# Performance work log

Hardware: AMD Instinct MI355X
Metric: run time of the kernel (lower is better)

Reference implementation:

```python
import jax, jax.numpy as jnp
import numpy as np

N_NODES = 100000
N_EDGES = 800000
IN_DIM, HID, OUT_DIM = 128, 96, 32
BN_EPS = 1e-5


def gcn_conv(x, W, b, src, dst, n):
    # PyG GCNConv: linear -> symmetric-normalized aggregation (with self-loops) -> +bias
    h = x @ W  # [N, out]
    sl = jnp.arange(n)
    s = jnp.concatenate([src, sl])
    d = jnp.concatenate([dst, sl])
    deg = jax.ops.segment_sum(jnp.ones(s.shape[0], dtype=x.dtype), d, num_segments=n)
    dinv = jnp.where(deg > 0, jax.lax.rsqrt(deg), 0.0)
    norm = dinv[s] * dinv[d]  # [E+N]
    out = jax.ops.segment_sum(norm[:, None] * h[s], d, num_segments=n)
    return out + b


def batchnorm(x, gamma, beta):
    mu = jnp.mean(x, axis=0)
    var = jnp.var(x, axis=0)
    return gamma * (x - mu) * jax.lax.rsqrt(var + BN_EPS) + beta


def setup_inputs() -> dict:
    key = jax.random.key(0)
    ks = jax.random.split(key, 8)
    glorot = lambda k, fi, fo: jax.random.normal(k, (fi, fo), jnp.float32) * np.sqrt(2.0 / (fi + fo))
    return {
        "x": jax.random.normal(ks[0], (N_NODES, IN_DIM), jnp.float32),
        "edge_index": jax.random.randint(ks[1], (2, N_EDGES), 0, N_NODES, jnp.int64),
        "W1": glorot(ks[2], IN_DIM, HID), "b1": jnp.zeros((HID,), jnp.float32),
        "W2": glorot(ks[3], HID, HID), "b2": jnp.zeros((HID,), jnp.float32),
        "W3": glorot(ks[4], HID, OUT_DIM), "b3": jnp.zeros((OUT_DIM,), jnp.float32),
        "g1": jnp.ones((HID,), jnp.float32), "be1": jnp.zeros((HID,), jnp.float32),
        "g2": jnp.ones((HID,), jnp.float32), "be2": jnp.zeros((HID,), jnp.float32),
    }


def reference(x, edge_index, W1, b1, W2, b2, W3, b3, g1, be1, g2, be2):
    src, dst = edge_index[0], edge_index[1]
    n = x.shape[0]
    h = gcn_conv(x, W1, b1, src, dst, n)
    h = jax.nn.relu(batchnorm(h, g1, be1))  # dropout is identity in eval
    h = gcn_conv(h, W2, b2, src, dst, n)
    h = jax.nn.relu(batchnorm(h, g2, be2))
    h = gcn_conv(h, W3, b3, src, dst, n)
    return jax.nn.log_softmax(h, axis=-1)
```

## Files before the change

### kernel.cpp

```cpp
#include <hip/hip_runtime.h>
#include <hip/hip_fp16.h>
#include <cstddef>

#define NN 100000
#define NE 800000
#define DIN 128
#define HID 96
#define DOUT 32
static constexpr float BN_EPS = 1e-5f;
#define SCAN_NB ((NN + 255) / 256)

typedef unsigned short u16;
typedef unsigned int u32;

__device__ __forceinline__ float b2f(u32 lo16) {
    union { u32 u; float f; } c; c.u = lo16 << 16; return c.f;
}
__device__ __forceinline__ u16 f2b(float f) {
    union { float f; u32 u; } c; c.f = f;
    return (u16)((c.u + 0x7FFFu + ((c.u >> 16) & 1u)) >> 16);
}
__device__ __forceinline__ u32 pack_edge(int s, float w) {
    __half h = __float2half(w);
    return ((u32)s << 15) | (u32)__half_as_ushort(h);
}
__device__ __forceinline__ int edge_src(u32 pk) { return (int)(pk >> 15); }
__device__ __forceinline__ float edge_wt(u32 pk) {
    return __half2float(__ushort_as_half((u16)(pk & 0x7FFFu)));
}


__global__ void k_init(int* __restrict__ deg) {
    int i = blockIdx.x * 256 + threadIdx.x;
    if (i < NN) deg[i] = 0;
}

__global__ __launch_bounds__(256) void k_scan1(const int* __restrict__ deg,
                                               int* __restrict__ row_start,
                                               int* __restrict__ blksum,
                                               float* __restrict__ dinv) {
    __shared__ int lds[256];
    int t = threadIdx.x;
    int i = blockIdx.x * 256 + t;
    int v = (i < NN) ? deg[i] : 0;
    if (i < NN) dinv[i] = rsqrtf((float)(v + 1));
    lds[t] = v;
    __syncthreads();
#pragma unroll
    for (int off = 1; off < 256; off <<= 1) {
        int add = (t >= off) ? lds[t - off] : 0;
        __syncthreads();
        lds[t] += add;
        __syncthreads();
    }
    if (i < NN) row_start[i] = lds[t] - v;
    if (t == 255) blksum[blockIdx.x] = lds[255];
}

__global__ __launch_bounds__(512) void k_scan2(int* __restrict__ blksum,
                                               int* __restrict__ row_start,
                                               float* __restrict__ meta) {
    __shared__ int lds[512];
    int t = threadIdx.x;
    if (t < 384) meta[t] = 0.f;
    int v = (t < SCAN_NB) ? blksum[t] : 0;
    lds[t] = v;
    __syncthreads();
#pragma unroll
    for (int off = 1; off < 512; off <<= 1) {
        int add = (t >= off) ? lds[t - off] : 0;
        __syncthreads();
        lds[t] += add;
        __syncthreads();
    }
    if (t < SCAN_NB) blksum[t] = lds[t] - v;
    if (t == 511) row_start[NN] = lds[511];
}

__global__ __launch_bounds__(256) void k_scan3(int* __restrict__ row_start,
                                               const int* __restrict__ blksum) {
    int i = blockIdx.x * 256 + threadIdx.x;
    if (i < NN) row_start[i] += blksum[blockIdx.x];
}

__global__ void k_scatter(const int* __restrict__ src, const int* __restrict__ dst,
                          const int* __restrict__ row_start,
                          const int* __restrict__ rank,
                          const float* __restrict__ dinv,
                          u32* __restrict__ ewt) {
    int e = blockIdx.x * blockDim.x + threadIdx.x;
    if (e < NE) {
        int d = dst[e];
        int p = row_start[d] + rank[e];
        int s = src[e];
        ewt[p] = pack_edge(s, dinv[s]);
    }
}

template <int KD, int ND, bool FUSE, typename XT>
__device__ __forceinline__ void gemm_body(int bid, const XT* __restrict__ X,
                                          const float* __restrict__ W,
                                          u16* __restrict__ Z,
                                          const float* __restrict__ bnA,
                                          const float* __restrict__ bnC, int M) {
    constexpr int BK = 32;
    constexpr int CT = 16;
    constexpr int CPT = ND / CT;
    constexpr int RPT = 8;
    constexpr int XS = 132;
    __shared__ float Xs[BK * XS];
    __shared__ float Ws[BK * ND];
    __shared__ float As[KD], Cs[KD];

    int tid = threadIdx.x;
    if (FUSE && tid < KD) { As[tid] = bnA[tid]; Cs[tid] = bnC[tid]; }
    int row0 = bid * 128;
    int ct = tid % CT, rt = tid / CT;
    float acc[RPT][CPT];
#pragma unroll
    for (int r = 0; r < RPT; ++r)
#pragma unroll
        for (int c = 0; c < CPT; ++c) acc[r][c] = 0.f;

    for (int k0 = 0; k0 < KD; k0 += BK) {
        __syncthreads();
        if constexpr (sizeof(XT) == 4) {
#pragma unroll
            for (int pass = 0; pass < 4; ++pass) {
                int r = pass * 32 + (tid >> 3);
                int kq = (tid & 7) * 4;
                int grow = row0 + r;
                float4 v = make_float4(0.f, 0.f, 0.f, 0.f);
                if (grow < M) v = *(const float4*)&X[(size_t)grow * KD + k0 + kq];
                if (FUSE) {
                    v.x = fmaxf(fmaf(As[k0 + kq + 0], v.x, Cs[k0 + kq + 0]), 0.f);
                    v.y = fmaxf(fmaf(As[k0 + kq + 1], v.y, Cs[k0 + kq + 1]), 0.f);
                    v.z = fmaxf(fmaf(As[k0 + kq + 2], v.z, Cs[k0 + kq + 2]), 0.f);
                    v.w = fmaxf(fmaf(As[k0 + kq + 3], v.w, Cs[k0 + kq + 3]), 0.f);
                }
                Xs[(kq + 0) * XS + r] = v.x;
                Xs[(kq + 1) * XS + r] = v.y;
                Xs[(kq + 2) * XS + r] = v.z;
                Xs[(kq + 3) * XS + r] = v.w;
            }
        } else {
#pragma unroll
            for (int pass = 0; pass < 2; ++pass) {
                int r = pass * 64 + (tid >> 2);
                int kq = (tid & 3) * 8;
                int grow = row0 + r;
                uint4 v = make_uint4(0, 0, 0, 0);
                if (grow < M) v = *(const uint4*)&X[(size_t)grow * KD + k0 + kq];
                u32 w[4] = {v.x, v.y, v.z, v.w};
#pragma unroll
                for (int q = 0; q < 4; ++q) {
                    float lo = b2f(w[q] & 0xFFFFu);
                    float hi = b2f(w[q] >> 16);
                    if (FUSE) {
                        lo = fmaxf(fmaf(As[k0 + kq + 2 * q + 0], lo, Cs[k0 + kq + 2 * q + 0]), 0.f);
                        hi = fmaxf(fmaf(As[k0 + kq + 2 * q + 1], hi, Cs[k0 + kq + 2 * q + 1]), 0.f);
                    }
                    Xs[(kq + 2 * q + 0) * XS + r] = lo;
                    Xs[(kq + 2 * q + 1) * XS + r] = hi;
                }
            }
        }
#pragma unroll
        for (int f = tid; f < BK * ND / 4; f += 256) {
            int kk = f / (ND / 4);
            int c4 = (f % (ND / 4)) * 4;
            *(float4*)&Ws[kk * ND + c4] = *(const float4*)&W[(size_t)(k0 + kk) * ND + c4];
        }
        __syncthreads();
#pragma unroll
        for (int kk = 0; kk < BK; ++kk) {
            float4 x0 = *(const float4*)&Xs[kk * XS + rt * 8];
            float4 x1 = *(const float4*)&Xs[kk * XS + rt * 8 + 4];
            float xr[RPT] = {x0.x, x0.y, x0.z, x0.w, x1.x, x1.y, x1.z, x1.w};
            float wc[CPT];
#pragma unroll
            for (int c = 0; c < CPT; ++c) wc[c] = Ws[kk * ND + ct * CPT + c];
#pragma unroll
            for (int r = 0; r < RPT; ++r)
#pragma unroll
                for (int c = 0; c < CPT; ++c) acc[r][c] = fmaf(xr[r], wc[c], acc[r][c]);
        }
    }
#pragma unroll
    for (int r = 0; r < RPT; ++r) {
        int grow = row0 + rt * RPT + r;
        if (grow < M) {
#pragma unroll
            for (int c = 0; c < CPT; c += 2) {
                u32 pk = (u32)f2b(acc[r][c]) | ((u32)f2b(acc[r][c + 1]) << 16);
                *(u32*)&Z[(size_t)grow * ND + ct * CPT + c] = pk;
            }
        }
    }
}

template <int KD, int ND, bool FUSE, typename XT>
__global__ __launch_bounds__(256) void k_gemm(const XT* __restrict__ X,
                                              const float* __restrict__ W,
                                              u16* __restrict__ Z,
                                              const float* __restrict__ bnA,
                                              const float* __restrict__ bnC, int M) {
    gemm_body<KD, ND, FUSE, XT>(blockIdx.x, X, W, Z, bnA, bnC, M);
}

__global__ __launch_bounds__(256) void k_gemm1_hist(const float* __restrict__ X,
                                                    const float* __restrict__ W,
                                                    u16* __restrict__ Z, int M,
                                                    int gemm_blocks,
                                                    const int* __restrict__ dst,
                                                    int* __restrict__ deg,
                                                    int* __restrict__ rank) {
    if ((int)blockIdx.x < gemm_blocks) {
        gemm_body<DIN, HID, false, float>(blockIdx.x, X, W, Z, nullptr, nullptr, M);
    } else {
        int e = ((int)blockIdx.x - gemm_blocks) * 256 + (int)threadIdx.x;
        if (e < NE) rank[e] = atomicAdd(&deg[dst[e]], 1);
    }
}

__global__ __launch_bounds__(256) void k_agg96(const u16* __restrict__ Z,
                                               u16* __restrict__ H,
                                               const float* __restrict__ bias,
                                               const int* __restrict__ row_start,
                                               const u32* __restrict__ ewt,
                                               const float* __restrict__ dinv,
                                               float* __restrict__ gsum,
                                               float* __restrict__ gsq) {
    __shared__ float ssum[96], ssq[96];
    int tid = threadIdx.x;
    if (tid < 96) { ssum[tid] = 0.f; ssq[tid] = 0.f; }
    __syncthreads();
    int wid = tid >> 6, lane = tid & 63;
    bool act = lane < 48;
    int l = act ? lane : 47;
    const u32* zu = (const u32*)Z;
    float b0 = bias[2 * l], b1 = bias[2 * l + 1];
    float lsum0 = 0.f, lsq0 = 0.f, lsum1 = 0.f, lsq1 = 0.f;
    const int stride = gridDim.x * 4;

    int n = blockIdx.x * 4 + wid;
    int e0 = 0, e1 = 0;
    u32 pr = 0;
    if (n < NN) {
        e0 = row_start[n]; e1 = row_start[n + 1];
        if (e0 + lane < e1) pr = ewt[e0 + lane];
    }
    while (n < NN) {
        int n2 = n + stride;
        int e0n = 0, e1n = 0;
        if (n2 < NN) { e0n = row_start[n2]; e1n = row_start[n2 + 1]; }

        float dn = dinv[n];
        u32 uself = zu[(size_t)n * 48 + l];
        float a0a = dn * b2f(uself & 0xFFFFu);
        float a1a = dn * b2f(uself >> 16);
        float a0b = 0.f, a1b = 0.f;

        u32 plv = pr;

        u32 prn = 0;
        if (n2 < NN && e0n + lane < e1n) prn = ewt[e0n + lane];

        int m = e1 - e0;
        if (m <= 64) {
            int K = (m + 7) >> 3;
            u32 uA[8], uB[8];
            float wA[8], wB[8];
            {
#pragma unroll
                for (int q = 0; q < 8; ++q) {
                    bool v = q < m;
                    u32 pk = __shfl(plv, v ? q : 0);
                    wA[q] = v ? edge_wt(pk) : 0.f;
                    uA[q] = zu[(size_t)edge_src(pk) * 48 + l];
                }
            }
            for (int c = 0; c < K; ++c) {
                if ((c & 1) == 0) {
                    if (c + 1 < K) {
#pragma unroll
                        for (int q = 0; q < 8; ++q) {
                            int j = (c + 1) * 8 + q;
                            bool v = j < m;
                            u32 pk = __shfl(plv, v ? j : 0);
                            wB[q] = v ? edge_wt(pk) : 0.f;
                            uB[q] = zu[(size_t)edge_src(pk) * 48 + l];
                        }
                    }
#pragma unroll
                    for (int q = 0; q < 8; q += 2) {
                        a0a = fmaf(wA[q], b2f(uA[q] & 0xFFFFu), a0a);
                        a1a = fmaf(wA[q], b2f(uA[q] >> 16), a1a);
                        a0b = fmaf(wA[q + 1], b2f(uA[q + 1] & 0xFFFFu), a0b);
                        a1b = fmaf(wA[q + 1], b2f(uA[q + 1] >> 16), a1b);
                    }
                } else {
                    if (c + 1 < K) {
#pragma unroll
                        for (int q = 0; q < 8; ++q) {
                            int j = (c + 1) * 8 + q;
                            bool v = j < m;
                            u32 pk = __shfl(plv, v ? j : 0);
                            wA[q] = v ? edge_wt(pk) : 0.f;
                            uA[q] = zu[(size_t)edge_src(pk) * 48 + l];
                        }
                    }
#pragma unroll
                    for (int q = 0; q < 8; q += 2) {
                        a0a = fmaf(wB[q], b2f(uB[q] & 0xFFFFu), a0a);
                        a1a = fmaf(wB[q], b2f(uB[q] >> 16), a1a);
                        a0b = fmaf(wB[q + 1], b2f(uB[q + 1] & 0xFFFFu), a0b);
                        a1b = fmaf(wB[q + 1], b2f(uB[q + 1] >> 16), a1b);
                    }
                }
            }
        } else {
            u32 cw = plv;
            for (int eb = e0; eb < e1; eb += 64) {
                if (eb != e0) {
                    int idx = eb + lane;
                    cw = (idx < e1) ? ewt[idx] : 0;
                }
                int mm = e1 - eb; if (mm > 64) mm = 64;
                for (int j = 0; j < mm; ++j) {
                    u32 pk = __shfl(cw, j);
                    float w = edge_wt(pk);
                    u32 u = zu[(size_t)edge_src(pk) * 48 + l];
                    a0a = fmaf(w, b2f(u & 0xFFFFu), a0a);
                    a1a = fmaf(w, b2f(u >> 16), a1a);
                }
            }
        }
        float h0 = fmaf(dn, a0a + a0b, b0);
        float h1 = fmaf(dn, a1a + a1b, b1);
        if (act) {
            u32 pk = (u32)f2b(h0) | ((u32)f2b(h1) << 16);
            ((u32*)H)[(size_t)n * 48 + l] = pk;
            lsum0 += h0; lsq0 = fmaf(h0, h0, lsq0);
            lsum1 += h1; lsq1 = fmaf(h1, h1, lsq1);
        }
        n = n2; e0 = e0n; e1 = e1n; pr = prn;
    }
    if (act) {
        atomicAdd(&ssum[2 * l], lsum0); atomicAdd(&ssq[2 * l], lsq0);
        atomicAdd(&ssum[2 * l + 1], lsum1); atomicAdd(&ssq[2 * l + 1], lsq1);
    }
    __syncthreads();
    if (tid < 96) { atomicAdd(&gsum[tid], ssum[tid]); atomicAdd(&gsq[tid], ssq[tid]); }
}

__global__ void k_bncoef(const float* __restrict__ gsum, const float* __restrict__ gsq,
                         const float* __restrict__ g, const float* __restrict__ be,
                         float* __restrict__ bnA, float* __restrict__ bnC) {
    int c = threadIdx.x;
    if (c < 96) {
        float mean = gsum[c] * (1.f / NN);
        float var = gsq[c] * (1.f / NN) - mean * mean;
        float inv = rsqrtf(var + BN_EPS);
        float a = g[c] * inv;
        bnA[c] = a;
        bnC[c] = fmaf(-a, mean, be[c]);
    }
}

__global__ __launch_bounds__(256) void k_agg32_lsm(const u16* __restrict__ Z,
                                                   float* __restrict__ Out,
                                                   const float* __restrict__ bias,
                                                   const int* __restrict__ row_start,
                                                   const u32* __restrict__ ewt,
                                                   const float* __restrict__ dinv) {
    int tid = threadIdx.x;
    int wid = tid >> 6, lane = tid & 63;
    int g = lane >> 4, sl = lane & 15;
    const u32* zu = (const u32*)Z;
    float b0 = bias[2 * sl], b1 = bias[2 * sl + 1];
    int stride = gridDim.x * 16;
    for (int n0 = (blockIdx.x * 4 + wid) * 4; n0 < NN; n0 += stride) {
        int n = n0 + g;
        bool vn = n < NN;
        float dn = vn ? dinv[n] : 0.f;
        u32 uself = vn ? zu[(size_t)n * 16 + sl] : 0;
        float a0a = dn * b2f(uself & 0xFFFFu);
        float a1a = dn * b2f(uself >> 16);
        float a0b = 0.f, a1b = 0.f;
        int e0 = vn ? row_start[n] : 0, e1 = vn ? row_start[n + 1] : 0;
        for (int eb = e0; eb < e1; eb += 16) {
            int m = e1 - eb; if (m > 16) m = 16;
            int idx = eb + sl;
            u32 plv = (idx < e1) ? ewt[idx] : 0;
            u32 u_[16]; float w_[16];
#pragma unroll
            for (int q = 0; q < 16; ++q) {
                bool v = q < m;
                u32 pk = __shfl(plv, v ? q : 0, 16);
                w_[q] = v ? edge_wt(pk) : 0.f;
                u_[q] = zu[(size_t)edge_src(pk) * 16 + sl];
            }
#pragma unroll
            for (int q = 0; q < 16; q += 2) {
                a0a = fmaf(w_[q], b2f(u_[q] & 0xFFFFu), a0a);
                a1a = fmaf(w_[q], b2f(u_[q] >> 16), a1a);
                a0b = fmaf(w_[q + 1], b2f(u_[q + 1] & 0xFFFFu), a0b);
                a1b = fmaf(w_[q + 1], b2f(u_[q + 1] >> 16), a1b);
            }
        }
        float v0 = fmaf(dn, a0a + a0b, b0);
        float v1 = fmaf(dn, a1a + a1b, b1);
        float mx = fmaxf(v0, v1);
#pragma unroll
        for (int off = 8; off; off >>= 1) mx = fmaxf(mx, __shfl_xor(mx, off, 16));
        float ex = __expf(v0 - mx) + __expf(v1 - mx);
#pragma unroll
        for (int off = 8; off; off >>= 1) ex += __shfl_xor(ex, off, 16);
        float lse = mx + __logf(ex);
        if (vn) {
            float2 o = make_float2(v0 - lse, v1 - lse);
            *(float2*)&Out[(size_t)n * 32 + 2 * sl] = o;
        }
    }
}


extern "C" void kernel_launch(void* const* d_in, const int* in_sizes, int n_in,
                              void* d_out, int out_size, void* d_ws, size_t ws_size,
                              hipStream_t stream) {
    const float* x  = (const float*)d_in[0];
    const int* ei   = (const int*)d_in[1];
    const float* W1 = (const float*)d_in[2];
    const float* b1 = (const float*)d_in[3];
    const float* W2 = (const float*)d_in[4];
    const float* b2 = (const float*)d_in[5];
    const float* W3 = (const float*)d_in[6];
    const float* b3 = (const float*)d_in[7];
    const float* g1 = (const float*)d_in[8];
    const float* be1 = (const float*)d_in[9];
    const float* g2 = (const float*)d_in[10];
    const float* be2 = (const float*)d_in[11];
    float* out = (float*)d_out;

    const int* src = ei;
    const int* dst = ei + NE;

    char* p = (char*)d_ws;
    size_t off = 0;
    auto take = [&](size_t bytes) {
        char* r = p + off;
        off = (off + bytes + 255) & ~(size_t)255;
        return r;
    };
    float* dinv      = (float*)take(NN * 4);
    int*   deg       = (int*)take(NN * 4);
    int*   row_start = (int*)take((NN + 1) * 4);
    int*   blksum    = (int*)take(SCAN_NB * 4);
    int*   rank      = (int*)take((size_t)NE * 4);
    u32*   ewt       = (u32*)take((size_t)NE * 4);
    float* meta      = (float*)take(768 * 4);
    u16*   bufA      = (u16*)take((size_t)NN * HID * 2);
    u16*   bufB      = (u16*)take((size_t)NN * HID * 2);

    float* sum1 = meta + 0,   *sq1 = meta + 96;
    float* sum2 = meta + 192, *sq2 = meta + 288;
    float* bnA1 = meta + 384, *bnC1 = meta + 480;
    float* bnA2 = meta + 576, *bnC2 = meta + 672;

    const int EB = (NE + 255) / 256;
    const int VB = (NN + 255) / 256;
    const int GB = (NN + 127) / 128;
    const int AB = 2048;

    k_init<<<VB, 256, 0, stream>>>(deg);
    k_gemm1_hist<<<GB + EB, 256, 0, stream>>>(x, W1, bufA, NN, GB, dst, deg, rank);
    k_scan1<<<SCAN_NB, 256, 0, stream>>>(deg, row_start, blksum, dinv);
    k_scan2<<<1, 512, 0, stream>>>(blksum, row_start, meta);
    k_scan3<<<SCAN_NB, 256, 0, stream>>>(row_start, blksum);
    k_scatter<<<EB, 256, 0, stream>>>(src, dst, row_start, rank, dinv, ewt);

    k_agg96<<<AB, 256, 0, stream>>>(bufA, bufB, b1, row_start, ewt, dinv, sum1, sq1);
    k_bncoef<<<1, 128, 0, stream>>>(sum1, sq1, g1, be1, bnA1, bnC1);

    k_gemm<HID, HID, true, u16><<<GB, 256, 0, stream>>>(bufB, W2, bufA, bnA1, bnC1, NN);
    k_agg96<<<AB, 256, 0, stream>>>(bufA, bufB, b2, row_start, ewt, dinv, sum2, sq2);
    k_bncoef<<<1, 128, 0, stream>>>(sum2, sq2, g2, be2, bnA2, bnC2);

    k_gemm<HID, DOUT, true, u16><<<GB, 256, 0, stream>>>(bufB, W3, bufA, bnA2, bnC2, NN);
    k_agg32_lsm<<<AB, 256, 0, stream>>>(bufA, out, b3, row_start, ewt, dinv);

    (void)in_sizes; (void)n_in; (void)out_size; (void)ws_size;
}
```

Baseline: 427.8 us.

## Fuse scan finalize into scatter, use nontemporal gather loads, chunk agg32 loop

Merges the third scan pass and the edge scatter into one launch, which writes finalized row offsets into a separate buffer while the scatter adds the block prefix itself. Edge-list and feature gathers in the aggregation kernels become nontemporal loads, meant to reduce cache pollution. The 32-wide aggregation now gathers in chunks of 8 with a dynamic trip count rather than a fixed 16-way unroll, cutting wasted loads on short rows. The risks are that nontemporal hints hurt the reuse of gathered rows that neighbouring nodes share, and that the 16-wide inner loop exposes less memory-level parallelism.

```diff
diff --git a/kernel.cpp b/kernel.cpp
--- a/kernel.cpp
+++ b/kernel.cpp
@@ -27,6 +27,9 @@
 __device__ __forceinline__ int edge_src(u32 pk) { return (int)(pk >> 15); }
 __device__ __forceinline__ float edge_wt(u32 pk) {
     return __half2float(__ushort_as_half((u16)(pk & 0x7FFFu)));
+}
+__device__ __forceinline__ u32 ntload(const u32* p) {
+    return __builtin_nontemporal_load(p);
 }
 
 
@@ -58,7 +61,6 @@
 }
 
 __global__ __launch_bounds__(512) void k_scan2(int* __restrict__ blksum,
-                                               int* __restrict__ row_start,
                                                float* __restrict__ meta) {
     __shared__ int lds[512];
     int t = threadIdx.x;
@@ -74,26 +76,30 @@
         __syncthreads();
     }
     if (t < SCAN_NB) blksum[t] = lds[t] - v;
-    if (t == 511) row_start[NN] = lds[511];
-}
-
-__global__ __launch_bounds__(256) void k_scan3(int* __restrict__ row_start,
-                                               const int* __restrict__ blksum) {
-    int i = blockIdx.x * 256 + threadIdx.x;
-    if (i < NN) row_start[i] += blksum[blockIdx.x];
-}
-
-__global__ void k_scatter(const int* __restrict__ src, const int* __restrict__ dst,
-                          const int* __restrict__ row_start,
-                          const int* __restrict__ rank,
-                          const float* __restrict__ dinv,
-                          u32* __restrict__ ewt) {
-    int e = blockIdx.x * blockDim.x + threadIdx.x;
-    if (e < NE) {
-        int d = dst[e];
-        int p = row_start[d] + rank[e];
-        int s = src[e];
-        ewt[p] = pack_edge(s, dinv[s]);
+}
+
+__global__ __launch_bounds__(256) void k_fin_scatter(const int* __restrict__ row_start,
+                                                     const int* __restrict__ blksum,
+                                                     int* __restrict__ row_fin,
+                                                     int fin_blocks,
+                                                     const int* __restrict__ src,
+                                                     const int* __restrict__ dst,
+                                                     const int* __restrict__ rank,
+                                                     const float* __restrict__ dinv,
+                                                     u32* __restrict__ ewt) {
+    int bid = (int)blockIdx.x;
+    if (bid < fin_blocks) {
+        int i = bid * 256 + (int)threadIdx.x;
+        if (i < NN) row_fin[i] = row_start[i] + blksum[i >> 8];
+        if (bid == 0 && threadIdx.x == 0) row_fin[NN] = NE;
+    } else {
+        int e = (bid - fin_blocks) * 256 + (int)threadIdx.x;
+        if (e < NE) {
+            int d = dst[e];
+            int p = row_start[d] + blksum[d >> 8] + rank[e];
+            int s = src[e];
+            ewt[p] = pack_edge(s, dinv[s]);
+        }
     }
 }
 
@@ -248,7 +254,7 @@
     u32 pr = 0;
     if (n < NN) {
         e0 = row_start[n]; e1 = row_start[n + 1];
-        if (e0 + lane < e1) pr = ewt[e0 + lane];
+        if (e0 + lane < e1) pr = ntload(&ewt[e0 + lane]);
     }
     while (n < NN) {
         int n2 = n + stride;
@@ -264,7 +270,7 @@
         u32 plv = pr;
 
         u32 prn = 0;
-        if (n2 < NN && e0n + lane < e1n) prn = ewt[e0n + lane];
+        if (n2 < NN && e0n + lane < e1n) prn = ntload(&ewt[e0n + lane]);
 
         int m = e1 - e0;
         if (m <= 64) {
@@ -277,7 +283,7 @@
                     bool v = q < m;
                     u32 pk = __shfl(plv, v ? q : 0);
                     wA[q] = v ? edge_wt(pk) : 0.f;
-                    uA[q] = zu[(size_t)edge_src(pk) * 48 + l];
+                    uA[q] = ntload(&zu[(size_t)edge_src(pk) * 48 + l]);
                 }
             }
             for (int c = 0; c < K; ++c) {
@@ -289,7 +295,7 @@
                             bool v = j < m;
                             u32 pk = __shfl(plv, v ? j : 0);
                             wB[q] = v ? edge_wt(pk) : 0.f;
-                            uB[q] = zu[(size_t)edge_src(pk) * 48 + l];
+                            uB[q] = ntload(&zu[(size_t)edge_src(pk) * 48 + l]);
                         }
                     }
 #pragma unroll
@@ -307,7 +313,7 @@
                             bool v = j < m;
                             u32 pk = __shfl(plv, v ? j : 0);
                             wA[q] = v ? edge_wt(pk) : 0.f;
-                            uA[q] = zu[(size_t)edge_src(pk) * 48 + l];
+                            uA[q] = ntload(&zu[(size_t)edge_src(pk) * 48 + l]);
                         }
                     }
 #pragma unroll
@@ -324,13 +330,13 @@
             for (int eb = e0; eb < e1; eb += 64) {
                 if (eb != e0) {
                     int idx = eb + lane;
-                    cw = (idx < e1) ? ewt[idx] : 0;
+                    cw = (idx < e1) ? ntload(&ewt[idx]) : 0;
                 }
                 int mm = e1 - eb; if (mm > 64) mm = 64;
                 for (int j = 0; j < mm; ++j) {
                     u32 pk = __shfl(cw, j);
                     float w = edge_wt(pk);
-                    u32 u = zu[(size_t)edge_src(pk) * 48 + l];
+                    u32 u = ntload(&zu[(size_t)edge_src(pk) * 48 + l]);
                     a0a = fmaf(w, b2f(u & 0xFFFFu), a0a);
                     a1a = fmaf(w, b2f(u >> 16), a1a);
                 }
@@ -390,23 +396,26 @@
         float a0b = 0.f, a1b = 0.f;
         int e0 = vn ? row_start[n] : 0, e1 = vn ? row_start[n + 1] : 0;
         for (int eb = e0; eb < e1; eb += 16) {
-            int m = e1 - eb; if (m > 16) m = 16;
+            int mm = e1 - eb; if (mm > 16) mm = 16;
             int idx = eb + sl;
-            u32 plv = (idx < e1) ? ewt[idx] : 0;
-            u32 u_[16]; float w_[16];
-#pragma unroll
-            for (int q = 0; q < 16; ++q) {
-                bool v = q < m;
-                u32 pk = __shfl(plv, v ? q : 0, 16);
-                w_[q] = v ? edge_wt(pk) : 0.f;
-                u_[q] = zu[(size_t)edge_src(pk) * 16 + sl];
-            }
-#pragma unroll
-            for (int q = 0; q < 16; q += 2) {
-                a0a = fmaf(w_[q], b2f(u_[q] & 0xFFFFu), a0a);
-                a1a = fmaf(w_[q], b2f(u_[q] >> 16), a1a);
-                a0b = fmaf(w_[q + 1], b2f(u_[q + 1] & 0xFFFFu), a0b);
-                a1b = fmaf(w_[q + 1], b2f(u_[q + 1] >> 16), a1b);
+            u32 plv = (idx < e1) ? ntload(&ewt[idx]) : 0;
+            for (int j = 0; j < mm; j += 8) {
+                int rem = mm - j; if (rem > 8) rem = 8;
+                u32 u_[8]; float w_[8];
+#pragma unroll
+                for (int q = 0; q < 8; ++q) {
+                    bool v = q < rem;
+                    u32 pk = __shfl(plv, j + (v ? q : 0), 16);
+                    w_[q] = v ? edge_wt(pk) : 0.f;
+                    u_[q] = ntload(&zu[(size_t)edge_src(pk) * 16 + sl]);
+                }
+#pragma unroll
+                for (int q = 0; q < 8; q += 2) {
+                    a0a = fmaf(w_[q], b2f(u_[q] & 0xFFFFu), a0a);
+                    a1a = fmaf(w_[q], b2f(u_[q] >> 16), a1a);
+                    a0b = fmaf(w_[q + 1], b2f(u_[q + 1] & 0xFFFFu), a0b);
+                    a1b = fmaf(w_[q + 1], b2f(u_[q + 1] >> 16), a1b);
+                }
             }
         }
         float v0 = fmaf(dn, a0a + a0b, b0);
@@ -456,6 +465,7 @@
     float* dinv      = (float*)take(NN * 4);
     int*   deg       = (int*)take(NN * 4);
     int*   row_start = (int*)take((NN + 1) * 4);
+    int*   row_fin   = (int*)take((NN + 1) * 4);
     int*   blksum    = (int*)take(SCAN_NB * 4);
     int*   rank      = (int*)take((size_t)NE * 4);
     u32*   ewt       = (u32*)take((size_t)NE * 4);
@@ -476,19 +486,19 @@
     k_init<<<VB, 256, 0, stream>>>(deg);
     k_gemm1_hist<<<GB + EB, 256, 0, stream>>>(x, W1, bufA, NN, GB, dst, deg, rank);
     k_scan1<<<SCAN_NB, 256, 0, stream>>>(deg, row_start, blksum, dinv);
-    k_scan2<<<1, 512, 0, stream>>>(blksum, row_start, meta);
-    k_scan3<<<SCAN_NB, 256, 0, stream>>>(row_start, blksum);
-    k_scatter<<<EB, 256, 0, stream>>>(src, dst, row_start, rank, dinv, ewt);
-
-    k_agg96<<<AB, 256, 0, stream>>>(bufA, bufB, b1, row_start, ewt, dinv, sum1, sq1);
+    k_scan2<<<1, 512, 0, stream>>>(blksum, meta);
+    k_fin_scatter<<<VB + EB, 256, 0, stream>>>(row_start, blksum, row_fin, VB,
+                                               src, dst, rank, dinv, ewt);
+
+    k_agg96<<<AB, 256, 0, stream>>>(bufA, bufB, b1, row_fin, ewt, dinv, sum1, sq1);
     k_bncoef<<<1, 128, 0, stream>>>(sum1, sq1, g1, be1, bnA1, bnC1);
 
     k_gemm<HID, HID, true, u16><<<GB, 256, 0, stream>>>(bufB, W2, bufA, bnA1, bnC1, NN);
-    k_agg96<<<AB, 256, 0, stream>>>(bufA, bufB, b2, row_start, ewt, dinv, sum2, sq2);
+    k_agg96<<<AB, 256, 0, stream>>>(bufA, bufB, b2, row_fin, ewt, dinv, sum2, sq2);
     k_bncoef<<<1, 128, 0, stream>>>(sum2, sq2, g2, be2, bnA2, bnC2);
 
     k_gemm<HID, DOUT, true, u16><<<GB, 256, 0, stream>>>(bufB, W3, bufA, bnA2, bnC2, NN);
-    k_agg32_lsm<<<AB, 256, 0, stream>>>(bufA, out, b3, row_start, ewt, dinv);
+    k_agg32_lsm<<<AB, 256, 0, stream>>>(bufA, out, b3, row_fin, ewt, dinv);
 
     (void)in_sizes; (void)n_in; (void)out_size; (void)ws_size;
 }
```

New measurement: 468.3 us. 9.5% more time.
